# Performance work log

Measured on AMD Instinct MI355X. Metric: run time of the kernel, lower is better.

## Reference

```python
import jax, jax.numpy as jnp
import numpy as np

B, S, H, V, E, C = 32, 512, 512, 32000, 768, 3
D = E + C  # LSTM input dim = embedding + one-hot prior


def setup_inputs() -> dict:
    key = jax.random.key(0)
    ks = jax.random.split(key, 13)
    p = lambda k, shape: (jax.random.normal(k, shape, jnp.float32) * 0.02)
    return {
        "embedding_table": p(ks[0], (V, E)),
        "fwd_kernel": p(ks[1], (D, 4 * H)),
        "fwd_rec_kernel": p(ks[2], (H, 4 * H)),
        "fwd_bias": p(ks[3], (4 * H,)),
        "bwd_kernel": p(ks[4], (D, 4 * H)),
        "bwd_rec_kernel": p(ks[5], (H, 4 * H)),
        "bwd_bias": p(ks[6], (4 * H,)),
        "w1": p(ks[7], (2 * H, H)),
        "b1": jnp.zeros((H,), jnp.float32),
        "w2": p(ks[8], (H, C)),
        "b2": jnp.zeros((C,), jnp.float32),
        "input_ids": jax.random.randint(ks[9], (B, S), 0, V),
        "prior_info": jax.random.randint(ks[10], (B, S), 0, C),
        "labels": jax.random.randint(ks[11], (B, S), 0, C),
    }


def _lstm(x, K, R, b, reverse):
    """Keras-style LSTM (gate order i,f,c,o). x: [B,S,D] -> [B,S,H].
    With reverse=True, lax.scan processes time backwards and emits outputs
    aligned to original positions, matching Keras Bidirectional's
    go_backwards + output re-reversal."""
    zx = jnp.einsum('bsd,dh->bsh', x, K) + b  # input projection, [B,S,4H]
    zx = jnp.swapaxes(zx, 0, 1)               # [S,B,4H]
    h0 = jnp.zeros((x.shape[0], R.shape[0]), x.dtype)

    def step(carry, z):
        h, c = carry
        z = z + h @ R
        i, f, g, o = jnp.split(z, 4, axis=-1)
        c = jax.nn.sigmoid(f) * c + jax.nn.sigmoid(i) * jnp.tanh(g)
        h = jax.nn.sigmoid(o) * jnp.tanh(c)
        return (h, c), h

    _, ys = jax.lax.scan(step, (h0, h0), zx, reverse=reverse)
    return jnp.swapaxes(ys, 0, 1)  # [B,S,H]


def reference(embedding_table, fwd_kernel, fwd_rec_kernel, fwd_bias,
              bwd_kernel, bwd_rec_kernel, bwd_bias,
              w1, b1, w2, b2, input_ids, prior_info, labels):
    emb = embedding_table[input_ids]                       # [B,S,E] gather
    prior = jax.nn.one_hot(prior_info, C, dtype=emb.dtype)  # [B,S,3]
    x = jnp.concatenate([emb, prior], axis=-1)             # [B,S,771]
    hf = _lstm(x, fwd_kernel, fwd_rec_kernel, fwd_bias, reverse=False)
    hb = _lstm(x, bwd_kernel, bwd_rec_kernel, bwd_bias, reverse=True)
    h = jnp.concatenate([hf, hb], axis=-1)                 # [B,S,2H]
    h = h @ w1 + b1                                        # Dense (linear)
    logits = h @ w2 + b2                                   # [B,S,3]
    probs = jax.nn.softmax(logits, axis=-1)
    logp = jax.nn.log_softmax(logits, axis=-1)
    lab = jax.nn.one_hot(labels, C, dtype=logp.dtype)
    loss = jnp.mean(-jnp.sum(logp * lab, axis=(-1, -2)))
    return probs, loss
```

## Files before the change

kernel.cpp:

```cpp
#include <hip/hip_runtime.h>
#include <hip/hip_bf16.h>

#define BB 32
#define SS 512
#define HH 512
#define VV 32000
#define EE 768
#define NC 3
#define G4 2048
#define MM (BB*SS)
#define SENT 0xFFFFFFFFu

typedef __attribute__((ext_vector_type(8))) short bf16x8;
typedef __attribute__((ext_vector_type(4))) float f32x4;
typedef unsigned int u32;
typedef unsigned short u16;
typedef unsigned long long u64;
typedef __attribute__((ext_vector_type(4))) u32 u32x4;
typedef __attribute__((ext_vector_type(2))) u32 u32x2;

#define MFMA(a,b,c) __builtin_amdgcn_mfma_f32_16x16x32_bf16(a,b,c,0,0,0)

static __device__ __forceinline__ u16 f2bf(float f) {
  union { float f; u32 u; } v; v.f = f;
  return (u16)((v.u + 0x7fffu + ((v.u >> 16) & 1u)) >> 16);
}
static __device__ __forceinline__ float bf2f(u16 h) {
  union { u32 u; float f; } v; v.u = ((u32)h) << 16;
  return v.f;
}
static __device__ __forceinline__ float sigm(float x) { return 1.f/(1.f+__expf(-x)); }
static __device__ __forceinline__ float tanh_f(float x) {
  x = fminf(8.f, fmaxf(-8.f, x));
  float t = __expf(2.f*x);
  return (t-1.f)/(t+1.f);
}

__global__ void k_conv(const float* __restrict__ src, u16* __restrict__ dst, int n8) {
  int i = blockIdx.x * blockDim.x + threadIdx.x;
  if (i >= n8) return;
  const float4* s = ((const float4*)src) + (size_t)i*2;
  float4 a = s[0], b = s[1];
  u32 x = (u32)f2bf(a.x) | ((u32)f2bf(a.y) << 16);
  u32 y = (u32)f2bf(a.z) | ((u32)f2bf(a.w) << 16);
  u32 z = (u32)f2bf(b.x) | ((u32)f2bf(b.y) << 16);
  u32 w = (u32)f2bf(b.z) | ((u32)f2bf(b.w) << 16);
  ((uint4*)dst)[i] = make_uint4(x, y, z, w);
}

__global__ void k_pack(const float* __restrict__ src, u16* __restrict__ dst, int K, int N) {
  int tid = blockIdx.x * 256 + threadIdx.x;
  int nkf = K >> 5;
  int l = tid & 63, fi = tid >> 6;
  int kf = fi % nkf, nf = fi / nkf;
  if (nf >= (N >> 4)) return;
  int col = nf * 16 + (l & 15);
  int k0 = kf * 32 + (l >> 4) * 8;
  u32 o[4];
  #pragma unroll
  for (int j = 0; j < 4; ++j) {
    u16 lo = f2bf(src[(size_t)(k0 + 2*j) * N + col]);
    u16 hi = f2bf(src[(size_t)(k0 + 2*j + 1) * N + col]);
    o[j] = (u32)lo | ((u32)hi << 16);
  }
  *((uint4*)(dst + (size_t)tid * 8)) = make_uint4(o[0], o[1], o[2], o[3]);
}

__global__ __launch_bounds__(256) void k_proj(
    const u16* __restrict__ embT, const u16* __restrict__ Bp0, const u16* __restrict__ Bp1,
    const float* __restrict__ bias0, const float* __restrict__ bias1,
    const float* __restrict__ K0, const float* __restrict__ K1,
    const int* __restrict__ ids, const int* __restrict__ prior,
    u16* __restrict__ zx0, u16* __restrict__ zx1)
{
  int mt = blockIdx.x;
  int gy = blockIdx.y;
  int dir = gy >> 4, nt = gy & 15;
  const u16* Bp = dir ? Bp1 : Bp0;
  const float* bias = dir ? bias1 : bias0;
  const float* Kp = (dir ? K1 : K0) + (size_t)EE * G4;
  u16* zx = dir ? zx1 : zx0;
  int w = threadIdx.x >> 6, l = threadIdx.x & 63;
  int m0 = mt * 128 + w * 32;
  int r0 = m0 + (l & 15);
  int id0 = ids[(r0 & 31) * SS + (r0 >> 5)];
  int id1 = ids[((r0 + 16) & 31) * SS + ((r0 + 16) >> 5)];
  const u16* a0p = embT + (size_t)id0 * EE + (l >> 4) * 8;
  const u16* a1p = embT + (size_t)id1 * EE + (l >> 4) * 8;
  f32x4 acc[2][8];
  #pragma unroll
  for (int i = 0; i < 2; ++i)
    #pragma unroll
    for (int j = 0; j < 8; ++j) acc[i][j] = (f32x4){0.f,0.f,0.f,0.f};
  const u16* bbase = Bp + ((size_t)(nt*8)*24)*512 + (size_t)l*8;
  for (int kf = 0; kf < 24; ++kf) {
    bf16x8 a0 = *(const bf16x8*)(a0p + kf*32);
    bf16x8 a1 = *(const bf16x8*)(a1p + kf*32);
    #pragma unroll
    for (int nf = 0; nf < 8; ++nf) {
      bf16x8 bv = *(const bf16x8*)(bbase + (size_t)(nf*24 + kf)*512);
      acc[0][nf] = MFMA(a0, bv, acc[0][nf]);
      acc[1][nf] = MFMA(a1, bv, acc[1][nf]);
    }
  }
  int cb = nt*128 + (l & 15);
  #pragma unroll
  for (int mi = 0; mi < 2; ++mi) {
    #pragma unroll
    for (int r = 0; r < 4; ++r) {
      int row = m0 + mi*16 + (l >> 4)*4 + r;
      int p = prior[(row & 31) * SS + (row >> 5)];
      const float* kr = Kp + (size_t)p * G4;
      u16* zr = zx + (size_t)row * G4;
      #pragma unroll
      for (int nf = 0; nf < 8; ++nf) {
        int col = cb + nf*16;
        zr[col] = f2bf(acc[mi][nf][r] + bias[col] + kr[col]);
      }
    }
  }
}

__global__ __launch_bounds__(256, 1) void k_scan(
    const u16* __restrict__ zxf, const u16* __restrict__ zxb,
    const u16* __restrict__ Rf, const u16* __restrict__ Rb,
    u16* __restrict__ hf, u16* __restrict__ hb)
{
  int wg = blockIdx.x, dir = wg >> 4, wgi = wg & 15;
  const u16* zx = dir ? zxb : zxf;
  const u16* Rp = dir ? Rb : Rf;
  u16* hbuf = dir ? hb : hf;
  int tid = threadIdx.x;
  int g = tid >> 6, l = tid & 63;
  int ncb0 = g*32 + wgi*2;
  bf16x8 rb0[16], rb1[16];
  #pragma unroll
  for (int kf = 0; kf < 16; ++kf) {
    rb0[kf] = *(const bf16x8*)(Rp + (((size_t)ncb0*16 + kf)*64 + l)*8);
    rb1[kf] = *(const bf16x8*)(Rp + (((size_t)(ncb0+1)*16 + kf)*64 + l)*8);
  }
  #pragma unroll
  for (int kf = 0; kf < 16; ++kf) {
    asm volatile("" : "+v"(rb0[kf]));
    asm volatile("" : "+v"(rb1[kf]));
  }

  __shared__ char hstage[32*1040];
  __shared__ float zbuf[4][32][33];

  int eb = tid >> 3;
  int ecb = (tid & 7) * 4;
  const char* sread0 = hstage + (l & 15)*1040 + (l >> 4)*16;
  const char* sread1 = sread0 + 16*1040;
  char* swrite = hstage + (tid >> 3)*1040 + (tid & 7)*16;
  size_t goff = (size_t)(tid >> 3)*1024 + (tid & 7)*16;

  float c0 = 0.f, c1 = 0.f, c2 = 0.f, c3 = 0.f;
  for (int step = 0; step < SS; ++step) {
    int t = dir ? (SS - 1 - step) : step;
    const u16* zxr = zx + ((size_t)t*BB + eb)*G4 + wgi*32 + ecb;
    u32x2 xi = *(const u32x2*)(zxr);
    u32x2 xf = *(const u32x2*)(zxr + 512);
    u32x2 xg = *(const u32x2*)(zxr + 1024);
    u32x2 xo = *(const u32x2*)(zxr + 1536);
    f32x4 a00 = {0.f,0.f,0.f,0.f}, a01 = {0.f,0.f,0.f,0.f};
    f32x4 a10 = {0.f,0.f,0.f,0.f}, a11 = {0.f,0.f,0.f,0.f};
    if (step > 0) {
      int tp = dir ? t + 1 : t - 1;
      const char* gsrc = (const char*)(hbuf + (size_t)tp*BB*HH) + goff;
      u32x4 S0, S1, S2, S3, S4, S5, S6, S7;
      #define LDC(r, off) asm volatile("global_load_dwordx4 %0, %1, off " off " sc0 sc1" \
                                       : "=v"(r) : "v"(gsrc) : "memory")
      for (;;) {
        LDC(S0, "");            LDC(S1, "offset:128");
        LDC(S2, "offset:256");  LDC(S3, "offset:384");
        LDC(S4, "offset:512");  LDC(S5, "offset:640");
        LDC(S6, "offset:768");  LDC(S7, "offset:896");
        asm volatile("s_waitcnt vmcnt(0)" ::: "memory");
        __builtin_amdgcn_sched_barrier(0);
        bool ok = S0[0]!=SENT && S0[1]!=SENT && S0[2]!=SENT && S0[3]!=SENT
               && S1[0]!=SENT && S1[1]!=SENT && S1[2]!=SENT && S1[3]!=SENT
               && S2[0]!=SENT && S2[1]!=SENT && S2[2]!=SENT && S2[3]!=SENT
               && S3[0]!=SENT && S3[1]!=SENT && S3[2]!=SENT && S3[3]!=SENT
               && S4[0]!=SENT && S4[1]!=SENT && S4[2]!=SENT && S4[3]!=SENT
               && S5[0]!=SENT && S5[1]!=SENT && S5[2]!=SENT && S5[3]!=SENT
               && S6[0]!=SENT && S6[1]!=SENT && S6[2]!=SENT && S6[3]!=SENT
               && S7[0]!=SENT && S7[1]!=SENT && S7[2]!=SENT && S7[3]!=SENT;
        if (__all(ok)) break;
        __builtin_amdgcn_s_sleep(1);
      }
      #undef LDC
      __builtin_amdgcn_sched_barrier(0);
      *(u32x4*)(swrite)       = S0;
      *(u32x4*)(swrite + 128) = S1;
      *(u32x4*)(swrite + 256) = S2;
      *(u32x4*)(swrite + 384) = S3;
      *(u32x4*)(swrite + 512) = S4;
      *(u32x4*)(swrite + 640) = S5;
      *(u32x4*)(swrite + 768) = S6;
      *(u32x4*)(swrite + 896) = S7;
      __syncthreads();
      #pragma unroll
      for (int kf = 0; kf < 16; ++kf) {
        bf16x8 f0 = *(const bf16x8*)(sread0 + kf*64);
        bf16x8 f1 = *(const bf16x8*)(sread1 + kf*64);
        a00 = MFMA(f0, rb0[kf], a00);
        a01 = MFMA(f0, rb1[kf], a01);
        a10 = MFMA(f1, rb0[kf], a10);
        a11 = MFMA(f1, rb1[kf], a11);
      }
    }
    int zc = l & 15;
    int zr = (l >> 4) * 4;
    #pragma unroll
    for (int r = 0; r < 4; ++r) {
      zbuf[g][zc][zr + r]           = a00[r];
      zbuf[g][16 + zc][zr + r]      = a01[r];
      zbuf[g][zc][16 + zr + r]      = a10[r];
      zbuf[g][16 + zc][16 + zr + r] = a11[r];
    }
    __syncthreads();
    float z0[4], z1[4], z2[4], z3[4];
    #pragma unroll
    for (int j = 0; j < 4; ++j) {
      z0[j] = zbuf[0][ecb + j][eb];
      z1[j] = zbuf[1][ecb + j][eb];
      z2[j] = zbuf[2][ecb + j][eb];
      z3[j] = zbuf[3][ecb + j][eb];
    }
    z0[0] += bf2f((u16)(xi[0] & 0xffffu)); z0[1] += bf2f((u16)(xi[0] >> 16));
    z0[2] += bf2f((u16)(xi[1] & 0xffffu)); z0[3] += bf2f((u16)(xi[1] >> 16));
    z1[0] += bf2f((u16)(xf[0] & 0xffffu)); z1[1] += bf2f((u16)(xf[0] >> 16));
    z1[2] += bf2f((u16)(xf[1] & 0xffffu)); z1[3] += bf2f((u16)(xf[1] >> 16));
    z2[0] += bf2f((u16)(xg[0] & 0xffffu)); z2[1] += bf2f((u16)(xg[0] >> 16));
    z2[2] += bf2f((u16)(xg[1] & 0xffffu)); z2[3] += bf2f((u16)(xg[1] >> 16));
    z3[0] += bf2f((u16)(xo[0] & 0xffffu)); z3[1] += bf2f((u16)(xo[0] >> 16));
    z3[2] += bf2f((u16)(xo[1] & 0xffffu)); z3[3] += bf2f((u16)(xo[1] >> 16));
    c0 = sigm(z1[0])*c0 + sigm(z0[0])*tanh_f(z2[0]);
    c1 = sigm(z1[1])*c1 + sigm(z0[1])*tanh_f(z2[1]);
    c2 = sigm(z1[2])*c2 + sigm(z0[2])*tanh_f(z2[2]);
    c3 = sigm(z1[3])*c3 + sigm(z0[3])*tanh_f(z2[3]);
    float h0 = sigm(z3[0])*tanh_f(c0);
    float h1 = sigm(z3[1])*tanh_f(c1);
    float h2 = sigm(z3[2])*tanh_f(c2);
    float h3 = sigm(z3[3])*tanh_f(c3);
    u32x2 hpk;
    hpk[0] = (u32)f2bf(h0) | ((u32)f2bf(h1) << 16);
    hpk[1] = (u32)f2bf(h2) | ((u32)f2bf(h3) << 16);
    u16* hp = hbuf + ((size_t)t*BB + eb)*HH + wgi*32 + ecb;
    asm volatile("global_store_dwordx2 %0, %1, off sc0 sc1" :: "v"(hp), "v"(hpk) : "memory");
  }
}

__global__ __launch_bounds__(256) void k_dense(
    const u16* __restrict__ hf, const u16* __restrict__ hb,
    const u16* __restrict__ w1p, const float* __restrict__ b1,
    u16* __restrict__ h1)
{
  int mt = blockIdx.x, nt = blockIdx.y;
  int w = threadIdx.x >> 6, l = threadIdx.x & 63;
  int m0 = mt*128 + w*32;
  int r0 = m0 + (l & 15);
  const u16* f0 = hf + (size_t)r0*HH + (l >> 4)*8;
  const u16* f1 = hf + (size_t)(r0+16)*HH + (l >> 4)*8;
  const u16* g0 = hb + (size_t)r0*HH + (l >> 4)*8;
  const u16* g1 = hb + (size_t)(r0+16)*HH + (l >> 4)*8;
  f32x4 acc[2][8];
  #pragma unroll
  for (int i = 0; i < 2; ++i)
    #pragma unroll
    for (int j = 0; j < 8; ++j) acc[i][j] = (f32x4){0.f,0.f,0.f,0.f};
  const u16* bbase = w1p + ((size_t)(nt*8)*32)*512 + (size_t)l*8;
  for (int kf = 0; kf < 32; ++kf) {
    const u16* s0 = (kf < 16) ? (f0 + kf*32) : (g0 + (kf-16)*32);
    const u16* s1 = (kf < 16) ? (f1 + kf*32) : (g1 + (kf-16)*32);
    bf16x8 a0 = *(const bf16x8*)s0;
    bf16x8 a1 = *(const bf16x8*)s1;
    #pragma unroll
    for (int nf = 0; nf < 8; ++nf) {
      bf16x8 bv = *(const bf16x8*)(bbase + (size_t)(nf*32 + kf)*512);
      acc[0][nf] = MFMA(a0, bv, acc[0][nf]);
      acc[1][nf] = MFMA(a1, bv, acc[1][nf]);
    }
  }
  int cb = nt*128 + (l & 15);
  #pragma unroll
  for (int mi = 0; mi < 2; ++mi) {
    #pragma unroll
    for (int r = 0; r < 4; ++r) {
      int row = m0 + mi*16 + (l >> 4)*4 + r;
      #pragma unroll
      for (int nf = 0; nf < 8; ++nf) {
        int col = cb + nf*16;
        h1[(size_t)row*HH + col] = f2bf(acc[mi][nf][r] + b1[col]);
      }
    }
  }
}

__global__ __launch_bounds__(256) void k_out(
    const u16* __restrict__ h1, const float* __restrict__ w2, const float* __restrict__ b2,
    const int* __restrict__ labels, float* __restrict__ out, float* __restrict__ part)
{
  int w = threadIdx.x >> 6, l = threadIdx.x & 63;
  float w2r[8][3];
  #pragma unroll
  for (int i = 0; i < 8; ++i)
    #pragma unroll
    for (int c = 0; c < 3; ++c) w2r[i][c] = w2[(l*8 + i)*3 + c];
  float b20 = b2[0], b21 = b2[1], b22 = b2[2];
  float nll = 0.f;
  int base = (blockIdx.x*4 + w)*16;
  for (int r = 0; r < 16; ++r) {
    int row = base + r;
    bf16x8 hv = *(const bf16x8*)(h1 + (size_t)row*HH + l*8);
    float s0 = 0.f, s1 = 0.f, s2 = 0.f;
    #pragma unroll
    for (int i = 0; i < 8; ++i) {
      float x = bf2f((u16)hv[i]);
      s0 += x*w2r[i][0]; s1 += x*w2r[i][1]; s2 += x*w2r[i][2];
    }
    #pragma unroll
    for (int off = 32; off > 0; off >>= 1) {
      s0 += __shfl_down(s0, off);
      s1 += __shfl_down(s1, off);
      s2 += __shfl_down(s2, off);
    }
    if (l == 0) {
      float l0 = s0+b20, l1 = s1+b21, l2 = s2+b22;
      float m = fmaxf(l0, fmaxf(l1, l2));
      float e0 = __expf(l0-m), e1 = __expf(l1-m), e2 = __expf(l2-m);
      float Z = e0+e1+e2, inv = 1.f/Z;
      int b = row & 31, s = row >> 5;
      float* po = out + ((size_t)b*SS + s)*3;
      po[0] = e0*inv; po[1] = e1*inv; po[2] = e2*inv;
      int lab = labels[b*SS + s];
      float ll = (lab == 0) ? l0 : (lab == 1 ? l1 : l2);
      nll += (m + __logf(Z)) - ll;
    }
  }
  __shared__ float ps[4];
  if (l == 0) ps[w] = nll;
  __syncthreads();
  if (threadIdx.x == 0) part[blockIdx.x] = ps[0]+ps[1]+ps[2]+ps[3];
}

__global__ void k_loss(const float* __restrict__ part, float* __restrict__ out) {
  __shared__ float sh[256];
  sh[threadIdx.x] = part[threadIdx.x];
  __syncthreads();
  for (int s = 128; s > 0; s >>= 1) {
    if (threadIdx.x < s) sh[threadIdx.x] += sh[threadIdx.x + s];
    __syncthreads();
  }
  if (threadIdx.x == 0) out[(size_t)MM*NC] = sh[0] / (float)BB;
}

extern "C" void kernel_launch(void* const* d_in, const int* in_sizes, int n_in,
                              void* d_out, int out_size, void* d_ws, size_t ws_size,
                              hipStream_t stream) {
  (void)in_sizes; (void)n_in; (void)out_size;
  const float* emb = (const float*)d_in[0];
  const float* fK  = (const float*)d_in[1];
  const float* fR  = (const float*)d_in[2];
  const float* fb  = (const float*)d_in[3];
  const float* bK  = (const float*)d_in[4];
  const float* bR  = (const float*)d_in[5];
  const float* bb  = (const float*)d_in[6];
  const float* w1  = (const float*)d_in[7];
  const float* b1  = (const float*)d_in[8];
  const float* w2  = (const float*)d_in[9];
  const float* b2  = (const float*)d_in[10];
  const int* ids   = (const int*)d_in[11];
  const int* prior = (const int*)d_in[12];
  const int* labels= (const int*)d_in[13];

  size_t off = 0;
  auto take = [&](size_t bytes) -> char* {
    char* p = (char*)d_ws + off;
    off += (bytes + 255) & ~(size_t)255;
    return p;
  };
  u16* embT = (u16*)take((size_t)VV*EE*2);
  u16* Kfp  = (u16*)take((size_t)EE*G4*2);
  u16* Kbp  = (u16*)take((size_t)EE*G4*2);
  u16* Rfp  = (u16*)take((size_t)HH*G4*2);
  u16* Rbp  = (u16*)take((size_t)HH*G4*2);
  u16* w1p  = (u16*)take((size_t)(2*HH)*HH*2);
  u16* zxf  = (u16*)take((size_t)MM*G4*2);
  u16* zxb  = (u16*)take((size_t)MM*G4*2);
  u16* hf   = (u16*)take((size_t)MM*HH*2);
  u16* hb   = (u16*)take((size_t)MM*HH*2);
  u16* h1   = (u16*)take((size_t)MM*HH*2);
  float* part = (float*)take(256*4);
  if (off > ws_size) return;

  hipMemsetAsync(hf, 0xFF, (size_t)MM*HH*2, stream);
  hipMemsetAsync(hb, 0xFF, (size_t)MM*HH*2, stream);
  k_conv<<<12000, 256, 0, stream>>>(emb, embT, VV*EE/8);
  k_pack<<<768, 256, 0, stream>>>(fK, Kfp, EE, G4);
  k_pack<<<768, 256, 0, stream>>>(bK, Kbp, EE, G4);
  k_pack<<<512, 256, 0, stream>>>(fR, Rfp, HH, G4);
  k_pack<<<512, 256, 0, stream>>>(bR, Rbp, HH, G4);
  k_pack<<<256, 256, 0, stream>>>(w1, w1p, 2*HH, HH);
  k_proj<<<dim3(128,32), 256, 0, stream>>>(embT, Kfp, Kbp, fb, bb, fK, bK, ids, prior, zxf, zxb);
  k_scan<<<32, 256, 0, stream>>>(zxf, zxb, Rfp, Rbp, hf, hb);
  k_dense<<<dim3(128,4), 256, 0, stream>>>(hf, hb, w1p, b1, h1);
  k_out<<<256, 256, 0, stream>>>(h1, w2, b2, labels, (float*)d_out, part);
  k_loss<<<1, 256, 0, stream>>>(part, (float*)d_out);
}
```

Baseline: 2.211 ms.

## Fuse input projection into scan kernel with sentinel-polled producer/consumer overlap

Merges the input projection GEMM and the recurrent scan into one persistent launch. 32 blocks run the scan while 224 blocks compute zx tiles, alternating from both sequence ends so the forward and backward scans get their timesteps early. The scan polls zx for a 0xFFFF sentinel set by a new memset, so the projection overlaps the serial recurrence instead of running before it. The risks are extra memsets over the large zx buffers, polling traffic, and a hang if a computed bf16 value happens to equal the sentinel bit pattern or if the scan blocks are not co-resident.

```diff
diff --git a/kernel.cpp b/kernel.cpp
--- a/kernel.cpp
+++ b/kernel.cpp
@@ -15,7 +15,6 @@
 typedef __attribute__((ext_vector_type(4))) float f32x4;
 typedef unsigned int u32;
 typedef unsigned short u16;
-typedef unsigned long long u64;
 typedef __attribute__((ext_vector_type(4))) u32 u32x4;
 typedef __attribute__((ext_vector_type(2))) u32 u32x2;
 
@@ -34,6 +33,9 @@
   x = fminf(8.f, fmaxf(-8.f, x));
   float t = __expf(2.f*x);
   return (t-1.f)/(t+1.f);
+}
+static __device__ __forceinline__ bool ok16(u32 v) {
+  return ((v & 0xFFFFu) != 0xFFFFu) && ((v >> 16) != 0xFFFFu);
 }
 
 __global__ void k_conv(const float* __restrict__ src, u16* __restrict__ dst, int n8) {
@@ -66,67 +68,84 @@
   *((uint4*)(dst + (size_t)tid * 8)) = make_uint4(o[0], o[1], o[2], o[3]);
 }
 
-__global__ __launch_bounds__(256) void k_proj(
-    const u16* __restrict__ embT, const u16* __restrict__ Bp0, const u16* __restrict__ Bp1,
-    const float* __restrict__ bias0, const float* __restrict__ bias1,
-    const float* __restrict__ K0, const float* __restrict__ K1,
+static __device__ __forceinline__ void proj_role(
+    int pid,
+    const u16* __restrict__ embT, const u16* __restrict__ Kfp, const u16* __restrict__ Kbp,
+    const float* __restrict__ fb, const float* __restrict__ bb,
+    const float* __restrict__ fK, const float* __restrict__ bK,
     const int* __restrict__ ids, const int* __restrict__ prior,
-    u16* __restrict__ zx0, u16* __restrict__ zx1)
+    u16* __restrict__ zxf, u16* __restrict__ zxb)
 {
-  int mt = blockIdx.x;
-  int gy = blockIdx.y;
-  int dir = gy >> 4, nt = gy & 15;
-  const u16* Bp = dir ? Bp1 : Bp0;
-  const float* bias = dir ? bias1 : bias0;
-  const float* Kp = (dir ? K1 : K0) + (size_t)EE * G4;
-  u16* zx = dir ? zx1 : zx0;
   int w = threadIdx.x >> 6, l = threadIdx.x & 63;
-  int m0 = mt * 128 + w * 32;
-  int r0 = m0 + (l & 15);
-  int id0 = ids[(r0 & 31) * SS + (r0 >> 5)];
-  int id1 = ids[((r0 + 16) & 31) * SS + ((r0 + 16) >> 5)];
-  const u16* a0p = embT + (size_t)id0 * EE + (l >> 4) * 8;
-  const u16* a1p = embT + (size_t)id1 * EE + (l >> 4) * 8;
-  f32x4 acc[2][8];
-  #pragma unroll
-  for (int i = 0; i < 2; ++i)
-    #pragma unroll
-    for (int j = 0; j < 8; ++j) acc[i][j] = (f32x4){0.f,0.f,0.f,0.f};
-  const u16* bbase = Bp + ((size_t)(nt*8)*24)*512 + (size_t)l*8;
-  for (int kf = 0; kf < 24; ++kf) {
-    bf16x8 a0 = *(const bf16x8*)(a0p + kf*32);
-    bf16x8 a1 = *(const bf16x8*)(a1p + kf*32);
-    #pragma unroll
-    for (int nf = 0; nf < 8; ++nf) {
-      bf16x8 bv = *(const bf16x8*)(bbase + (size_t)(nf*24 + kf)*512);
-      acc[0][nf] = MFMA(a0, bv, acc[0][nf]);
-      acc[1][nf] = MFMA(a1, bv, acc[1][nf]);
-    }
-  }
-  int cb = nt*128 + (l & 15);
-  #pragma unroll
-  for (int mi = 0; mi < 2; ++mi) {
-    #pragma unroll
-    for (int r = 0; r < 4; ++r) {
-      int row = m0 + mi*16 + (l >> 4)*4 + r;
-      int p = prior[(row & 31) * SS + (row >> 5)];
-      const float* kr = Kp + (size_t)p * G4;
-      u16* zr = zx + (size_t)row * G4;
+  for (int wk = pid; wk < 4096; wk += 224) {
+    int kk = wk >> 5, gy = wk & 31;
+    int mt = (kk & 1) ? (127 - (kk >> 1)) : (kk >> 1);
+    int dir = gy >> 4, nt = gy & 15;
+    const u16* Bp = dir ? Kbp : Kfp;
+    const float* bias = dir ? bb : fb;
+    const float* Kp = (dir ? bK : fK) + (size_t)EE * G4;
+    u16* zx = dir ? zxb : zxf;
+    int m0 = mt * 128 + w * 32;
+    int r0 = m0 + (l & 15);
+    int id0 = ids[(r0 & 31) * SS + (r0 >> 5)];
+    int id1 = ids[((r0 + 16) & 31) * SS + ((r0 + 16) >> 5)];
+    const u16* a0p = embT + (size_t)id0 * EE + (l >> 4) * 8;
+    const u16* a1p = embT + (size_t)id1 * EE + (l >> 4) * 8;
+    f32x4 acc[2][8];
+    #pragma unroll
+    for (int i = 0; i < 2; ++i)
+      #pragma unroll
+      for (int j = 0; j < 8; ++j) acc[i][j] = (f32x4){0.f,0.f,0.f,0.f};
+    const u16* bbase = Bp + ((size_t)(nt*8)*24)*512 + (size_t)l*8;
+    for (int kf = 0; kf < 24; ++kf) {
+      bf16x8 a0 = *(const bf16x8*)(a0p + kf*32);
+      bf16x8 a1 = *(const bf16x8*)(a1p + kf*32);
       #pragma unroll
       for (int nf = 0; nf < 8; ++nf) {
-        int col = cb + nf*16;
-        zr[col] = f2bf(acc[mi][nf][r] + bias[col] + kr[col]);
-      }
-    }
-  }
-}
-
-__global__ __launch_bounds__(256, 1) void k_scan(
-    const u16* __restrict__ zxf, const u16* __restrict__ zxb,
+        bf16x8 bv = *(const bf16x8*)(bbase + (size_t)(nf*24 + kf)*512);
+        acc[0][nf] = MFMA(a0, bv, acc[0][nf]);
+        acc[1][nf] = MFMA(a1, bv, acc[1][nf]);
+      }
+    }
+    int cb = nt*128 + (l & 15);
+    #pragma unroll
+    for (int mi = 0; mi < 2; ++mi) {
+      #pragma unroll
+      for (int r = 0; r < 4; ++r) {
+        int row = m0 + mi*16 + (l >> 4)*4 + r;
+        int p = prior[(row & 31) * SS + (row >> 5)];
+        const float* kr = Kp + (size_t)p * G4;
+        u16* zr = zx + (size_t)row * G4;
+        #pragma unroll
+        for (int nf = 0; nf < 8; ++nf) {
+          int col = cb + nf*16;
+          u32 v = (u32)f2bf(acc[mi][nf][r] + bias[col] + kr[col]);
+          asm volatile("global_store_short %0, %1, off sc0 sc1"
+                       :: "v"(zr + col), "v"(v) : "memory");
+        }
+      }
+    }
+  }
+}
+
+__global__ __launch_bounds__(256, 1) void k_fused(
+    const u16* __restrict__ embT, const u16* __restrict__ Kfp, const u16* __restrict__ Kbp,
+    const float* __restrict__ fb, const float* __restrict__ bb,
+    const float* __restrict__ fK, const float* __restrict__ bK,
+    const int* __restrict__ ids, const int* __restrict__ prior,
+    u16* __restrict__ zxf, u16* __restrict__ zxb,
     const u16* __restrict__ Rf, const u16* __restrict__ Rb,
     u16* __restrict__ hf, u16* __restrict__ hb)
 {
-  int wg = blockIdx.x, dir = wg >> 4, wgi = wg & 15;
+  __shared__ char hstage[32*1040];
+  __shared__ float zbuf[4][32][33];
+
+  int wg = blockIdx.x;
+  if (wg >= 32) {
+    proj_role(wg - 32, embT, Kfp, Kbp, fb, bb, fK, bK, ids, prior, zxf, zxb);
+    return;
+  }
+  int dir = wg >> 4, wgi = wg & 15;
   const u16* zx = dir ? zxb : zxf;
   const u16* Rp = dir ? Rb : Rf;
   u16* hbuf = dir ? hb : hf;
@@ -139,14 +158,6 @@
     rb0[kf] = *(const bf16x8*)(Rp + (((size_t)ncb0*16 + kf)*64 + l)*8);
     rb1[kf] = *(const bf16x8*)(Rp + (((size_t)(ncb0+1)*16 + kf)*64 + l)*8);
   }
-  #pragma unroll
-  for (int kf = 0; kf < 16; ++kf) {
-    asm volatile("" : "+v"(rb0[kf]));
-    asm volatile("" : "+v"(rb1[kf]));
-  }
-
-  __shared__ char hstage[32*1040];
-  __shared__ float zbuf[4][32][33];
 
   int eb = tid >> 3;
   int ecb = (tid & 7) * 4;
@@ -158,11 +169,10 @@
   float c0 = 0.f, c1 = 0.f, c2 = 0.f, c3 = 0.f;
   for (int step = 0; step < SS; ++step) {
     int t = dir ? (SS - 1 - step) : step;
-    const u16* zxr = zx + ((size_t)t*BB + eb)*G4 + wgi*32 + ecb;
-    u32x2 xi = *(const u32x2*)(zxr);
-    u32x2 xf = *(const u32x2*)(zxr + 512);
-    u32x2 xg = *(const u32x2*)(zxr + 1024);
-    u32x2 xo = *(const u32x2*)(zxr + 1536);
+    const char* zxp = (const char*)(zx + ((size_t)t*BB + eb)*G4 + wgi*32 + ecb);
+    u32x2 xi, xfv, xgv, xov;
+    #define LDZ(r, off) asm volatile("global_load_dwordx2 %0, %1, off " off " sc0 sc1" \
+                                     : "=v"(r) : "v"(zxp) : "memory")
     f32x4 a00 = {0.f,0.f,0.f,0.f}, a01 = {0.f,0.f,0.f,0.f};
     f32x4 a10 = {0.f,0.f,0.f,0.f}, a11 = {0.f,0.f,0.f,0.f};
     if (step > 0) {
@@ -172,13 +182,17 @@
       #define LDC(r, off) asm volatile("global_load_dwordx4 %0, %1, off " off " sc0 sc1" \
                                        : "=v"(r) : "v"(gsrc) : "memory")
       for (;;) {
+        LDZ(xi, "");  LDZ(xfv, "offset:1024");
+        LDZ(xgv, "offset:2048"); LDZ(xov, "offset:3072");
         LDC(S0, "");            LDC(S1, "offset:128");
         LDC(S2, "offset:256");  LDC(S3, "offset:384");
         LDC(S4, "offset:512");  LDC(S5, "offset:640");
         LDC(S6, "offset:768");  LDC(S7, "offset:896");
         asm volatile("s_waitcnt vmcnt(0)" ::: "memory");
         __builtin_amdgcn_sched_barrier(0);
-        bool ok = S0[0]!=SENT && S0[1]!=SENT && S0[2]!=SENT && S0[3]!=SENT
+        bool ok = ok16(xi[0]) && ok16(xi[1]) && ok16(xfv[0]) && ok16(xfv[1])
+               && ok16(xgv[0]) && ok16(xgv[1]) && ok16(xov[0]) && ok16(xov[1])
+               && S0[0]!=SENT && S0[1]!=SENT && S0[2]!=SENT && S0[3]!=SENT
                && S1[0]!=SENT && S1[1]!=SENT && S1[2]!=SENT && S1[3]!=SENT
                && S2[0]!=SENT && S2[1]!=SENT && S2[2]!=SENT && S2[3]!=SENT
                && S3[0]!=SENT && S3[1]!=SENT && S3[2]!=SENT && S3[3]!=SENT
@@ -209,7 +223,20 @@
         a10 = MFMA(f1, rb0[kf], a10);
         a11 = MFMA(f1, rb1[kf], a11);
       }
-    }
+    } else {
+      for (;;) {
+        LDZ(xi, "");  LDZ(xfv, "offset:1024");
+        LDZ(xgv, "offset:2048"); LDZ(xov, "offset:3072");
+        asm volatile("s_waitcnt vmcnt(0)" ::: "memory");
+        __builtin_amdgcn_sched_barrier(0);
+        bool ok = ok16(xi[0]) && ok16(xi[1]) && ok16(xfv[0]) && ok16(xfv[1])
+               && ok16(xgv[0]) && ok16(xgv[1]) && ok16(xov[0]) && ok16(xov[1]);
+        if (__all(ok)) break;
+        __builtin_amdgcn_s_sleep(1);
+      }
+      __builtin_amdgcn_sched_barrier(0);
+    }
+    #undef LDZ
     int zc = l & 15;
     int zr = (l >> 4) * 4;
     #pragma unroll
@@ -230,12 +257,12 @@
     }
     z0[0] += bf2f((u16)(xi[0] & 0xffffu)); z0[1] += bf2f((u16)(xi[0] >> 16));
     z0[2] += bf2f((u16)(xi[1] & 0xffffu)); z0[3] += bf2f((u16)(xi[1] >> 16));
-    z1[0] += bf2f((u16)(xf[0] & 0xffffu)); z1[1] += bf2f((u16)(xf[0] >> 16));
-    z1[2] += bf2f((u16)(xf[1] & 0xffffu)); z1[3] += bf2f((u16)(xf[1] >> 16));
-    z2[0] += bf2f((u16)(xg[0] & 0xffffu)); z2[1] += bf2f((u16)(xg[0] >> 16));
-    z2[2] += bf2f((u16)(xg[1] & 0xffffu)); z2[3] += bf2f((u16)(xg[1] >> 16));
-    z3[0] += bf2f((u16)(xo[0] & 0xffffu)); z3[1] += bf2f((u16)(xo[0] >> 16));
-    z3[2] += bf2f((u16)(xo[1] & 0xffffu)); z3[3] += bf2f((u16)(xo[1] >> 16));
+    z1[0] += bf2f((u16)(xfv[0] & 0xffffu)); z1[1] += bf2f((u16)(xfv[0] >> 16));
+    z1[2] += bf2f((u16)(xfv[1] & 0xffffu)); z1[3] += bf2f((u16)(xfv[1] >> 16));
+    z2[0] += bf2f((u16)(xgv[0] & 0xffffu)); z2[1] += bf2f((u16)(xgv[0] >> 16));
+    z2[2] += bf2f((u16)(xgv[1] & 0xffffu)); z2[3] += bf2f((u16)(xgv[1] >> 16));
+    z3[0] += bf2f((u16)(xov[0] & 0xffffu)); z3[1] += bf2f((u16)(xov[0] >> 16));
+    z3[2] += bf2f((u16)(xov[1] & 0xffffu)); z3[3] += bf2f((u16)(xov[1] >> 16));
     c0 = sigm(z1[0])*c0 + sigm(z0[0])*tanh_f(z2[0]);
     c1 = sigm(z1[1])*c1 + sigm(z0[1])*tanh_f(z2[1]);
     c2 = sigm(z1[2])*c2 + sigm(z0[2])*tanh_f(z2[2]);
@@ -395,6 +422,8 @@
   float* part = (float*)take(256*4);
   if (off > ws_size) return;
 
+  hipMemsetAsync(zxf, 0xFF, (size_t)MM*G4*2, stream);
+  hipMemsetAsync(zxb, 0xFF, (size_t)MM*G4*2, stream);
   hipMemsetAsync(hf, 0xFF, (size_t)MM*HH*2, stream);
   hipMemsetAsync(hb, 0xFF, (size_t)MM*HH*2, stream);
   k_conv<<<12000, 256, 0, stream>>>(emb, embT, VV*EE/8);
@@ -403,8 +432,8 @@
   k_pack<<<512, 256, 0, stream>>>(fR, Rfp, HH, G4);
   k_pack<<<512, 256, 0, stream>>>(bR, Rbp, HH, G4);
   k_pack<<<256, 256, 0, stream>>>(w1, w1p, 2*HH, HH);
-  k_proj<<<dim3(128,32), 256, 0, stream>>>(embT, Kfp, Kbp, fb, bb, fK, bK, ids, prior, zxf, zxb);
-  k_scan<<<32, 256, 0, stream>>>(zxf, zxb, Rfp, Rbp, hf, hb);
+  k_fused<<<256, 256, 0, stream>>>(embT, Kfp, Kbp, fb, bb, fK, bK, ids, prior,
+                                   zxf, zxb, Rfp, Rbp, hf, hb);
   k_dense<<<dim3(128,4), 256, 0, stream>>>(hf, hb, w1p, b1, h1);
   k_out<<<256, 256, 0, stream>>>(h1, w2, b2, labels, (float*)d_out, part);
   k_loss<<<1, 256, 0, stream>>>(part, (float*)d_out);
```

Measured after the change: 2.249 ms. No clear change (+1.7%).
